# Kernel tuning notes

Measured on AMD Instinct MI355X. Metric: run time of the kernel, lower is better.

Reference implementation:

```python
import jax, jax.numpy as jnp
import numpy as np

# Model constants (match init_kwargs)
H, P, N, G, NL, K = 32, 64, 128, 1, 15, 4   # heads, head_dim, state, groups, lambda levels, conv width
HID, T, BATCH = 1024, 1024, 1
INTER = H * P                    # 2048
CONV_DIM = INTER + 2 * G * N     # 2304
PROJ = INTER + CONV_DIM + H * (NL + 1)  # 4864
EPS = 1e-5


def _level_matrix(t_len: int) -> np.ndarray:
    """Fenwick-tree level assignment: for query t, prefix [0,t] splits into
    power-of-two segments from binary expansion of t+1; segment of length 2^l -> level l."""
    lm = np.zeros((t_len, t_len), dtype=np.int32)
    for t in range(t_len):
        n = t + 1
        while n > 0:
            lb = n & (-n)
            lm[t, n - lb:n] = lb.bit_length() - 1
            n -= lb
    return lm


def setup_inputs() -> dict:
    key = jax.random.key(0)
    ks = jax.random.split(key, 4)
    return {
        "hidden_states": jax.random.normal(ks[0], (BATCH, T, HID), jnp.float32),
        "in_proj_w": jax.random.normal(ks[1], (PROJ, HID), jnp.float32) / np.sqrt(HID).astype(np.float32),
        "in_proj_b": jnp.zeros((PROJ,), jnp.float32),
        "conv_w": jax.random.normal(ks[2], (CONV_DIM, K), jnp.float32) / np.sqrt(K).astype(np.float32),
        "dt_bias": jnp.ones((H,), jnp.float32),
        "A_log": jnp.log(jnp.arange(1, H + 1, dtype=jnp.float32)),
        "L_param": jnp.ones((H, NL), jnp.float32),
        "D": jnp.ones((H,), jnp.float32),
        "rmsnorm_w": jnp.ones((INTER,), jnp.float32),
        "out_proj_w": jax.random.normal(ks[3], (HID, INTER), jnp.float32) / np.sqrt(INTER).astype(np.float32),
        "out_proj_b": jnp.zeros((HID,), jnp.float32),
        "level_mat": jnp.asarray(_level_matrix(T)),  # (T,T) int32, data-independent
    }


def reference(hidden_states, in_proj_w, in_proj_b, conv_w, dt_bias, A_log,
              L_param, D, rmsnorm_w, out_proj_w, out_proj_b, level_mat):
    b, t, _ = hidden_states.shape
    # in_proj and split: [z | xBC | dt | dl]
    zxbcdtdl = hidden_states @ in_proj_w.T + in_proj_b
    z, xBC, dt, dl = jnp.split(zxbcdtdl, [INTER, INTER + CONV_DIM, INTER + CONV_DIM + H], axis=-1)
    # depthwise causal conv1d (width K) + SiLU
    xp = jnp.pad(xBC, ((0, 0), (K - 1, 0), (0, 0)))
    conv = sum(xp[:, w:w + t, :] * conv_w[:, w] for w in range(K))
    xBC = jax.nn.silu(conv)
    x, Bm, Cm = jnp.split(xBC, [INTER, INTER + G * N], axis=-1)
    x = x.reshape(b, t, H, P)          # v pre-scale
    Bm = Bm.reshape(b, t, G, N)        # keys
    Cm = Cm.reshape(b, t, G, N)        # queries
    dl = dl.reshape(b, t, H, NL)
    # D residual uses unscaled x (matches hmamba_chunk_scan_combined ordering)
    D_res = x * D[None, None, :, None]
    dt = jax.nn.softplus(dt + dt_bias)            # (b,t,H)
    v = x * dt[..., None]                          # (b,t,H,P)
    A = -jnp.exp(A_log)                            # (H,)
    g = A * dt                                     # (b,t,H), per-token log-decay (<=0)
    Ls = jax.nn.softplus(L_param * dl)             # (b,t,H,NL) per-token level scales
    # cumulative log-decay; decay(t,s) = exp(cg_t - cg_s), s<=t
    cg = jnp.cumsum(g, axis=1).transpose(0, 2, 1)  # (b,H,t)
    mask = jnp.tril(jnp.ones((t, t), bool))
    logdecay = jnp.where(mask, cg[:, :, :, None] - cg[:, :, None, :], -jnp.inf)
    decay = jnp.exp(logdecay)                      # (b,H,t,s)
    # hierarchical level scale H[t,s] = Ls[b,t,h, level(t,s)]
    Hmat = jnp.take_along_axis(Ls.transpose(0, 2, 1, 3), level_mat[None, None, :, :], axis=-1)  # (b,H,t,s)
    scores = jnp.einsum('btgn,bsgn->bgts', Cm, Bm)  # (b,G,t,s), G=1 broadcasts over heads
    att = scores * decay * Hmat                     # (b,H,t,s), masked via decay=0
    y = jnp.einsum('bhts,bshp->bthp', att, v) + D_res
    y = y.reshape(b, t, INTER)
    # gated RMSNorm with norm_before_gate=False: normalize(y * silu(z)) * w
    yg = y * jax.nn.silu(z)
    y = yg * jax.lax.rsqrt(jnp.mean(yg * yg, axis=-1, keepdims=True) + EPS) * rmsnorm_w
    return y @ out_proj_w.T + out_proj_b
```

## Files before the change

kernel.cpp:

```cpp
#include <hip/hip_runtime.h>
#include <hip/hip_bf16.h>
#include <math.h>

#define T_LEN 1024
#define HID 1024
#define NHEAD 32
#define HDIM 64
#define NSTATE 128
#define NLVL 15
#define KCONV 4
#define INTER 2048
#define CONV_DIM 2304
#define PROJ 4864
#define EPS 1e-5f

typedef __attribute__((ext_vector_type(8))) _Float16 half8;
typedef __attribute__((ext_vector_type(4))) float float4v;
typedef unsigned short ushort_t;

__device__ __forceinline__ float softplus_f(float x) {
  return fmaxf(x, 0.f) + log1pf(expf(-fabsf(x)));
}
__device__ __forceinline__ float silu_f(float x) {
  return x / (1.f + expf(-x));
}
__device__ __forceinline__ ushort_t f2h(float f) {
  union { _Float16 h; ushort_t u; } v;
  v.h = (_Float16)f;
  return v.u;
}
__device__ __forceinline__ void gload_lds16(const void* g, void* l) {
  __builtin_amdgcn_global_load_lds(
      (const __attribute__((address_space(1))) void*)g,
      (__attribute__((address_space(3))) void*)l, 16, 0, 0);
}

__global__ __launch_bounds__(256) void f32_to_f16(const float* __restrict__ src,
                                                  ushort_t* __restrict__ dst, int n4) {
  int i = blockIdx.x * 256 + threadIdx.x;
  if (i >= n4) return;
  float4 v = reinterpret_cast<const float4*>(src)[i];
  union { ushort_t u[4]; unsigned long long ll; } o;
  o.u[0] = f2h(v.x); o.u[1] = f2h(v.y); o.u[2] = f2h(v.z); o.u[3] = f2h(v.w);
  reinterpret_cast<unsigned long long*>(dst)[i] = o.ll;
}

__global__ __launch_bounds__(256) void gemm_f16_sk(
    const ushort_t* __restrict__ A, const ushort_t* __restrict__ B,
    float* __restrict__ Cpart, int M, int N, int K, int Kc) {
  __shared__ ushort_t As[2][128][32];
  __shared__ ushort_t Bs[2][128][32];
  const int tid = threadIdx.x;
  const int w = tid >> 6, L = tid & 63;
  const int n0 = blockIdx.x * 128, m0 = blockIdx.y * 128;
  const int kbeg = blockIdx.z * Kc;
  float* __restrict__ C = Cpart + (size_t)blockIdx.z * M * N;
  const int mq = (w & 1) * 64, nq = (w >> 1) * 64;

  const int srow = (L >> 2);
  const int sch = (L & 3) * 8;

  float4v acc[4][4];
#pragma unroll
  for (int i = 0; i < 4; ++i)
#pragma unroll
    for (int j = 0; j < 4; ++j) acc[i][j] = (float4v){0.f, 0.f, 0.f, 0.f};

  const int niter = Kc / 32;
  {
    const int kk = kbeg;
#pragma unroll
    for (int j = 0; j < 2; ++j) {
      int r0 = 16 * (w * 2 + j);
      gload_lds16(A + (size_t)(m0 + r0 + srow) * K + kk + sch, &As[0][r0][0]);
      gload_lds16(B + (size_t)(n0 + r0 + srow) * K + kk + sch, &Bs[0][r0][0]);
    }
  }
  for (int it = 0; it < niter; ++it) {
    __syncthreads();
    if (it + 1 < niter) {
      const int kk = kbeg + (it + 1) * 32;
      const int nb = (it + 1) & 1;
#pragma unroll
      for (int j = 0; j < 2; ++j) {
        int r0 = 16 * (w * 2 + j);
        gload_lds16(A + (size_t)(m0 + r0 + srow) * K + kk + sch, &As[nb][r0][0]);
        gload_lds16(B + (size_t)(n0 + r0 + srow) * K + kk + sch, &Bs[nb][r0][0]);
      }
    }
    const int cb = it & 1;
    half8 af[4], bf[4];
#pragma unroll
    for (int t = 0; t < 4; ++t) {
      af[t] = *reinterpret_cast<const half8*>(&As[cb][mq + t * 16 + (L & 15)][(L >> 4) * 8]);
      bf[t] = *reinterpret_cast<const half8*>(&Bs[cb][nq + t * 16 + (L & 15)][(L >> 4) * 8]);
    }
#pragma unroll
    for (int mt = 0; mt < 4; ++mt)
#pragma unroll
      for (int nt = 0; nt < 4; ++nt)
        acc[mt][nt] = __builtin_amdgcn_mfma_f32_16x16x32_f16(af[mt], bf[nt], acc[mt][nt], 0, 0, 0);
  }
  const int qrow = (L >> 4) * 4;
#pragma unroll
  for (int mt = 0; mt < 4; ++mt) {
#pragma unroll
    for (int nt = 0; nt < 4; ++nt) {
      int col = n0 + nq + nt * 16 + (L & 15);
#pragma unroll
      for (int r = 0; r < 4; ++r) {
        int row = m0 + mq + mt * 16 + qrow + r;
        C[(size_t)row * N + col] = acc[mt][nt][r];
      }
    }
  }
}

__global__ __launch_bounds__(256) void reduce_out4(const float* __restrict__ p,
                                                   const float* __restrict__ bias,
                                                   float* __restrict__ out, int MN) {
  int i = blockIdx.x * 256 + threadIdx.x;
  if (i * 4 >= MN) return;
  float4 a = reinterpret_cast<const float4*>(p)[i];
  float4 b = reinterpret_cast<const float4*>(p + MN)[i];
  float4 c = reinterpret_cast<const float4*>(p + 2 * (size_t)MN)[i];
  float4 d = reinterpret_cast<const float4*>(p + 3 * (size_t)MN)[i];
  int col = (i * 4) & (HID - 1);
  float4 bv = *reinterpret_cast<const float4*>(bias + col);
  float4 o;
  o.x = a.x + b.x + c.x + d.x + bv.x;
  o.y = a.y + b.y + c.y + d.y + bv.y;
  o.z = a.z + b.z + c.z + d.z + bv.z;
  o.w = a.w + b.w + c.w + d.w + bv.w;
  reinterpret_cast<float4*>(out)[i] = o;
}

__global__ __launch_bounds__(512) void pointwise_dt(
    const float* __restrict__ zx0, const float* __restrict__ zx1,
    const float* __restrict__ in_b, const float* __restrict__ dt_bias,
    const float* __restrict__ A_log, const float* __restrict__ L_param,
    float* __restrict__ dtbuf, float* __restrict__ gbuf,
    float* __restrict__ Lsbuf) {
  const int t = blockIdx.x;
  const int j = threadIdx.x;
  const size_t ro = (size_t)t * PROJ;
  if (j < NHEAD * NLVL) {
    int c = INTER + CONV_DIM + NHEAD + j;
    float x = L_param[j] * (zx0[ro + c] + zx1[ro + c] + in_b[c]);
    Lsbuf[(size_t)t * (NHEAD * NLVL) + j] = softplus_f(x);
  } else {
    int h = j - NHEAD * NLVL;
    int c = INTER + CONV_DIM + h;
    float x = zx0[ro + c] + zx1[ro + c] + in_b[c] + dt_bias[h];
    float dt = softplus_f(x);
    dtbuf[t * NHEAD + h] = dt;
    gbuf[t * NHEAD + h] = -expf(A_log[h]) * dt;
  }
}

__global__ __launch_bounds__(256) void conv_silu(
    const float* __restrict__ zx0, const float* __restrict__ zx1,
    const float* __restrict__ in_b, const float* __restrict__ conv_w,
    const float* __restrict__ dtbuf, const float* __restrict__ Dp,
    ushort_t* __restrict__ vb, float* __restrict__ ybuf,
    ushort_t* __restrict__ Bb, ushort_t* __restrict__ Cb) {
  int idx = blockIdx.x * 256 + threadIdx.x;
  if (idx >= T_LEN * CONV_DIM) return;
  int t = idx / CONV_DIM;
  int c = idx - t * CONV_DIM;
  const float bc = in_b[INTER + c];
  float acc = 0.f;
#pragma unroll
  for (int w = 0; w < KCONV; ++w) {
    int tt = t - (KCONV - 1) + w;
    if (tt >= 0) {
      size_t o = (size_t)tt * PROJ + INTER + c;
      acc += (zx0[o] + zx1[o] + bc) * conv_w[c * KCONV + w];
    }
  }
  float sil = silu_f(acc);
  if (c < INTER) {
    int h = c >> 6;
    float dt = dtbuf[t * NHEAD + h];
    vb[(size_t)t * INTER + c] = f2h(sil * dt);
    ybuf[(size_t)t * INTER + c] = sil * Dp[h];
  } else if (c < INTER + NSTATE) {
    Bb[t * NSTATE + (c - INTER)] = f2h(sil);
  } else {
    Cb[t * NSTATE + (c - INTER - NSTATE)] = f2h(sil);
  }
}

__global__ __launch_bounds__(256) void vtrans(const ushort_t* __restrict__ vb,
                                              ushort_t* __restrict__ vt) {
  __shared__ ushort_t Tl[64][72];
  const int tid = threadIdx.x;
  const int t0 = blockIdx.x * 64, c0 = blockIdx.y * 64;
#pragma unroll
  for (int i = 0; i < 2; ++i) {
    int u = tid + 256 * i;
    int r = u >> 3, c8 = (u & 7) * 8;
    *reinterpret_cast<half8*>(&Tl[r][c8]) =
        *reinterpret_cast<const half8*>(vb + (size_t)(t0 + r) * INTER + c0 + c8);
  }
  __syncthreads();
#pragma unroll
  for (int i = 0; i < 2; ++i) {
    int u = tid + 256 * i;
    int p = u >> 3, t8 = (u & 7) * 8;
    union { ushort_t u16[8]; half8 h; } o;
#pragma unroll
    for (int j = 0; j < 8; ++j) o.u16[j] = Tl[t8 + j][p];
    *reinterpret_cast<half8*>(vt + (size_t)(c0 + p) * T_LEN + t0 + t8) = o.h;
  }
}

__global__ __launch_bounds__(1024) void scan_g(const float* __restrict__ gbuf,
                                               double* __restrict__ cgd) {
  __shared__ double buf[T_LEN];
  const int h = blockIdx.x, t = threadIdx.x;
  buf[t] = (double)gbuf[t * NHEAD + h];
  __syncthreads();
  for (int off = 1; off < T_LEN; off <<= 1) {
    double v = buf[t];
    double a = (t >= off) ? buf[t - off] : 0.0;
    __syncthreads();
    buf[t] = v + a;
    __syncthreads();
  }
  cgd[(size_t)h * T_LEN + t] = buf[t];
}

__global__ __launch_bounds__(256) void attn_mfma(
    const ushort_t* __restrict__ Bb, const ushort_t* __restrict__ Cb,
    const ushort_t* __restrict__ vt, const double* __restrict__ cgd,
    const float* __restrict__ Lsb, float* __restrict__ ybuf) {
  __shared__ ushort_t Bl[64][136];
  __shared__ ushort_t Vtl[64][72];
  __shared__ ushort_t Sl[64][72];
  __shared__ float Lsl[64][17];
  __shared__ float cgq[64];
  __shared__ float cgs[64];

  const int item = blockIdx.x;
  const int h = item / 40;
  const int rem = item - h * 40;
  int qt, j;
  if (rem < 4)        { qt = rem;                 j = 0; }
  else if (rem < 12)  { qt = 4 + (rem - 4) / 2;   j = (rem - 4) % 2; }
  else if (rem < 24)  { qt = 8 + (rem - 12) / 3;  j = (rem - 12) % 3; }
  else                { qt = 12 + (rem - 24) / 4; j = (rem - 24) % 4; }

  const int tid = threadIdx.x;
  const int w = tid >> 6, L = tid & 63;
  const int tq0 = qt * 64;
  const double* cgh = cgd + (size_t)h * T_LEN;
  const double base = cgh[tq0];

  for (int i = tid; i < 64 * NLVL; i += 256) {
    int r = i / NLVL, l = i - r * NLVL;
    Lsl[r][l] = Lsb[(size_t)(tq0 + r) * (NHEAD * NLVL) + h * NLVL + l];
  }
  if (tid < 64) cgq[tid] = (float)(cgh[tq0 + tid] - base);

  half8 cfrag[4];
  {
    const ushort_t* cr = Cb + (size_t)(tq0 + w * 16 + (L & 15)) * NSTATE + (L >> 4) * 8;
#pragma unroll
    for (int ks = 0; ks < 4; ++ks)
      cfrag[ks] = *reinterpret_cast<const half8*>(cr + ks * 32);
  }
  float4v yac[4];
#pragma unroll
  for (int i = 0; i < 4; ++i) yac[i] = (float4v){0.f, 0.f, 0.f, 0.f};

  const int qrow = w * 16 + ((L >> 4) << 2);

  const int st0 = 4 * j;
  const int st1 = min(4 * j + 4, qt + 1);
  for (int st = st0; st < st1; ++st) {
    const int ts0 = st * 64;
    __syncthreads();
#pragma unroll
    for (int i = 0; i < 4; ++i) {
      int u = tid + 256 * i;
      int row = u >> 4, kb = (u & 15) * 8;
      *reinterpret_cast<half8*>(&Bl[row][kb]) =
          *reinterpret_cast<const half8*>(Bb + (size_t)(ts0 + row) * NSTATE + kb);
    }
#pragma unroll
    for (int i = 0; i < 2; ++i) {
      int u = tid + 256 * i;
      int p = u >> 3, sc = (u & 7) * 8;
      *reinterpret_cast<half8*>(&Vtl[p][sc]) =
          *reinterpret_cast<const half8*>(vt + (size_t)(h * HDIM + p) * T_LEN + ts0 + sc);
    }
    if (tid < 64) cgs[tid] = (float)(cgh[ts0 + tid] - base);
    __syncthreads();

    float4v sac[4];
#pragma unroll
    for (int nt = 0; nt < 4; ++nt) sac[nt] = (float4v){0.f, 0.f, 0.f, 0.f};
#pragma unroll
    for (int ks = 0; ks < 4; ++ks) {
#pragma unroll
      for (int nt = 0; nt < 4; ++nt) {
        half8 bfrag = *reinterpret_cast<const half8*>(&Bl[nt * 16 + (L & 15)][ks * 32 + (L >> 4) * 8]);
        sac[nt] = __builtin_amdgcn_mfma_f32_16x16x32_f16(cfrag[ks], bfrag, sac[nt], 0, 0, 0);
      }
    }
#pragma unroll
    for (int nt = 0; nt < 4; ++nt) {
      int s = nt * 16 + (L & 15);
      int sg = ts0 + s;
      float cs = cgs[s];
#pragma unroll
      for (int r = 0; r < 4; ++r) {
        int q = qrow + r;
        int tg = tq0 + q;
        float val = 0.f;
        if (sg <= tg) {
          int lvl = 31 - __clz((unsigned)(sg ^ (tg + 1)));
          val = sac[nt][r] * __expf(cgq[q] - cs) * Lsl[q][lvl];
        }
        Sl[q][s] = f2h(val);
      }
    }
    __builtin_amdgcn_s_waitcnt(0);
#pragma unroll
    for (int ks = 0; ks < 2; ++ks) {
      half8 af = *reinterpret_cast<const half8*>(&Sl[w * 16 + (L & 15)][ks * 32 + (L >> 4) * 8]);
#pragma unroll
      for (int pt = 0; pt < 4; ++pt) {
        half8 bfv = *reinterpret_cast<const half8*>(&Vtl[pt * 16 + (L & 15)][ks * 32 + (L >> 4) * 8]);
        yac[pt] = __builtin_amdgcn_mfma_f32_16x16x32_f16(af, bfv, yac[pt], 0, 0, 0);
      }
    }
  }
#pragma unroll
  for (int pt = 0; pt < 4; ++pt) {
    int p = pt * 16 + (L & 15);
#pragma unroll
    for (int r = 0; r < 4; ++r) {
      int q = qrow + r;
      atomicAdd(ybuf + (size_t)(tq0 + q) * INTER + h * HDIM + p, yac[pt][r]);
    }
  }
}

__global__ __launch_bounds__(256) void rmsnorm_gate(
    const float* __restrict__ ybuf, const float* __restrict__ zx0,
    const float* __restrict__ zx1, const float* __restrict__ in_b,
    const float* __restrict__ w, ushort_t* __restrict__ yhf) {
  __shared__ float red[4];
  const int t = blockIdx.x, tid = threadIdx.x;
  const size_t ro = (size_t)t * PROJ;
  const float* yrow = ybuf + (size_t)t * INTER;
  float yg[8];
  float ss = 0.f;
#pragma unroll
  for (int i = 0; i < 8; ++i) {
    int c = tid + 256 * i;
    float z = zx0[ro + c] + zx1[ro + c] + in_b[c];
    float g = yrow[c] * silu_f(z);
    yg[i] = g;
    ss += g * g;
  }
#pragma unroll
  for (int off = 32; off; off >>= 1) ss += __shfl_down(ss, off, 64);
  if ((tid & 63) == 0) red[tid >> 6] = ss;
  __syncthreads();
  if (tid == 0) red[0] = red[0] + red[1] + red[2] + red[3];
  __syncthreads();
  const float scale = rsqrtf(red[0] / (float)INTER + EPS);
#pragma unroll
  for (int i = 0; i < 8; ++i) {
    int c = tid + 256 * i;
    yhf[(size_t)t * INTER + c] = f2h(yg[i] * scale * w[c]);
  }
}

extern "C" void kernel_launch(void* const* d_in, const int* in_sizes, int n_in,
                              void* d_out, int out_size, void* d_ws, size_t ws_size,
                              hipStream_t stream) {
  const float* hs        = (const float*)d_in[0];
  const float* in_proj_w = (const float*)d_in[1];
  const float* in_proj_b = (const float*)d_in[2];
  const float* conv_w    = (const float*)d_in[3];
  const float* dt_bias   = (const float*)d_in[4];
  const float* A_log     = (const float*)d_in[5];
  const float* L_param   = (const float*)d_in[6];
  const float* Dp        = (const float*)d_in[7];
  const float* rms_w     = (const float*)d_in[8];
  const float* out_proj_w= (const float*)d_in[9];
  const float* out_proj_b= (const float*)d_in[10];
  float* out = (float*)d_out;

  char* W = (char*)d_ws;
  size_t off = 0;
  auto alloc = [&](size_t bytes) { void* p = W + off; off = (off + bytes + 255) & ~(size_t)255; return p; };
  double*   cgd = (double*)  alloc((size_t)NHEAD * T_LEN * 8);
  float*    zx0 = (float*)   alloc((size_t)T_LEN * PROJ * 4);
  float*    zx1 = (float*)   alloc((size_t)T_LEN * PROJ * 4);
  float*    opp = (float*)   alloc((size_t)4 * T_LEN * HID * 4);
  float*    ybuf= (float*)   alloc((size_t)T_LEN * INTER * 4);
  float*    gbuf= (float*)   alloc((size_t)T_LEN * NHEAD * 4);
  float*    dtb = (float*)   alloc((size_t)T_LEN * NHEAD * 4);
  float*    Lsb = (float*)   alloc((size_t)T_LEN * NHEAD * NLVL * 4);
  ushort_t* hsb = (ushort_t*)alloc((size_t)T_LEN * HID * 2);
  ushort_t* Wib = (ushort_t*)alloc((size_t)PROJ * HID * 2);
  ushort_t* Wob = (ushort_t*)alloc((size_t)HID * INTER * 2);
  ushort_t* yhf = (ushort_t*)alloc((size_t)T_LEN * INTER * 2);
  ushort_t* vb  = (ushort_t*)alloc((size_t)T_LEN * INTER * 2);
  ushort_t* vt  = (ushort_t*)alloc((size_t)T_LEN * INTER * 2);
  ushort_t* Bb  = (ushort_t*)alloc((size_t)T_LEN * NSTATE * 2);
  ushort_t* Cb  = (ushort_t*)alloc((size_t)T_LEN * NSTATE * 2);

  f32_to_f16<<<(T_LEN * HID / 4 + 255) / 256, 256, 0, stream>>>(hs, hsb, T_LEN * HID / 4);
  f32_to_f16<<<(PROJ * HID / 4 + 255) / 256, 256, 0, stream>>>(in_proj_w, Wib, PROJ * HID / 4);
  f32_to_f16<<<(HID * INTER / 4 + 255) / 256, 256, 0, stream>>>(out_proj_w, Wob, HID * INTER / 4);

  gemm_f16_sk<<<dim3(PROJ / 128, T_LEN / 128, 2), 256, 0, stream>>>(
      hsb, Wib, zx0, T_LEN, PROJ, HID, HID / 2);

  pointwise_dt<<<T_LEN, 512, 0, stream>>>(zx0, zx1, in_proj_b, dt_bias, A_log, L_param,
                                          dtb, gbuf, Lsb);

  conv_silu<<<(T_LEN * CONV_DIM + 255) / 256, 256, 0, stream>>>(
      zx0, zx1, in_proj_b, conv_w, dtb, Dp, vb, ybuf, Bb, Cb);

  vtrans<<<dim3(T_LEN / 64, INTER / 64), 256, 0, stream>>>(vb, vt);

  scan_g<<<NHEAD, T_LEN, 0, stream>>>(gbuf, cgd);

  attn_mfma<<<NHEAD * 40, 256, 0, stream>>>(Bb, Cb, vt, cgd, Lsb, ybuf);

  rmsnorm_gate<<<T_LEN, 256, 0, stream>>>(ybuf, zx0, zx1, in_proj_b, rms_w, yhf);

  gemm_f16_sk<<<dim3(HID / 128, T_LEN / 128, 4), 256, 0, stream>>>(
      yhf, Wob, opp, T_LEN, HID, INTER, INTER / 4);
  reduce_out4<<<(T_LEN * HID / 4 + 255) / 256, 256, 0, stream>>>(
      opp, out_proj_b, out, T_LEN * HID);
}
```

Before: 211.3 us.

## Fuse f16 conversions, fold V transpose into conv, and rewrite scan as wavefront

```diff
diff --git a/kernel.cpp b/kernel.cpp
--- a/kernel.cpp
+++ b/kernel.cpp
@@ -35,14 +35,22 @@
       (__attribute__((address_space(3))) void*)l, 16, 0, 0);
 }
 
-__global__ __launch_bounds__(256) void f32_to_f16(const float* __restrict__ src,
-                                                  ushort_t* __restrict__ dst, int n4) {
+#define N4_HS  (T_LEN * HID / 4)
+#define N4_WI  (PROJ * HID / 4)
+#define N4_WO  (HID * INTER / 4)
+__global__ __launch_bounds__(256) void prep_f16(
+    const float* __restrict__ hs, const float* __restrict__ wi,
+    const float* __restrict__ wo, ushort_t* __restrict__ hsb,
+    ushort_t* __restrict__ wib, ushort_t* __restrict__ wob) {
   int i = blockIdx.x * 256 + threadIdx.x;
-  if (i >= n4) return;
-  float4 v = reinterpret_cast<const float4*>(src)[i];
+  const float* src; ushort_t* dst; int j;
+  if (i < N4_HS)              { src = hs; dst = hsb; j = i; }
+  else if (i < N4_HS + N4_WI) { src = wi; dst = wib; j = i - N4_HS; }
+  else                        { src = wo; dst = wob; j = i - N4_HS - N4_WI; }
+  float4 v = reinterpret_cast<const float4*>(src)[j];
   union { ushort_t u[4]; unsigned long long ll; } o;
   o.u[0] = f2h(v.x); o.u[1] = f2h(v.y); o.u[2] = f2h(v.z); o.u[3] = f2h(v.w);
-  reinterpret_cast<unsigned long long*>(dst)[i] = o.ll;
+  reinterpret_cast<unsigned long long*>(dst)[j] = o.ll;
 }
 
 __global__ __launch_bounds__(256) void gemm_f16_sk(
@@ -56,7 +64,6 @@
   const int kbeg = blockIdx.z * Kc;
   float* __restrict__ C = Cpart + (size_t)blockIdx.z * M * N;
   const int mq = (w & 1) * 64, nq = (w >> 1) * 64;
-
   const int srow = (L >> 2);
   const int sch = (L & 3) * 8;
 
@@ -139,7 +146,7 @@
     const float* __restrict__ zx0, const float* __restrict__ zx1,
     const float* __restrict__ in_b, const float* __restrict__ dt_bias,
     const float* __restrict__ A_log, const float* __restrict__ L_param,
-    float* __restrict__ dtbuf, float* __restrict__ gbuf,
+    float* __restrict__ dtbuf, float* __restrict__ gT,
     float* __restrict__ Lsbuf) {
   const int t = blockIdx.x;
   const int j = threadIdx.x;
@@ -154,81 +161,90 @@
     float x = zx0[ro + c] + zx1[ro + c] + in_b[c] + dt_bias[h];
     float dt = softplus_f(x);
     dtbuf[t * NHEAD + h] = dt;
-    gbuf[t * NHEAD + h] = -expf(A_log[h]) * dt;
-  }
-}
-
-__global__ __launch_bounds__(256) void conv_silu(
+    gT[h * T_LEN + t] = -expf(A_log[h]) * dt;
+  }
+}
+
+__global__ __launch_bounds__(64) void scan_g(const float* __restrict__ gT,
+                                             double* __restrict__ cgd) {
+  const int h = blockIdx.x, l = threadIdx.x;
+  const float* gr = gT + (size_t)h * T_LEN + l * 16;
+  double pre[16];
+  double acc = 0.0;
+#pragma unroll
+  for (int i = 0; i < 16; ++i) { acc += (double)gr[i]; pre[i] = acc; }
+  double s = acc;
+#pragma unroll
+  for (int off = 1; off < 64; off <<= 1) {
+    double o = __shfl_up(s, off, 64);
+    if (l >= off) s += o;
+  }
+  const double base = s - acc;
+  double* cr = cgd + (size_t)h * T_LEN + l * 16;
+#pragma unroll
+  for (int i = 0; i < 16; ++i) cr[i] = base + pre[i];
+}
+
+__global__ __launch_bounds__(256) void conv_fused(
     const float* __restrict__ zx0, const float* __restrict__ zx1,
     const float* __restrict__ in_b, const float* __restrict__ conv_w,
     const float* __restrict__ dtbuf, const float* __restrict__ Dp,
-    ushort_t* __restrict__ vb, float* __restrict__ ybuf,
+    ushort_t* __restrict__ vt, float* __restrict__ ybuf,
     ushort_t* __restrict__ Bb, ushort_t* __restrict__ Cb) {
-  int idx = blockIdx.x * 256 + threadIdx.x;
-  if (idx >= T_LEN * CONV_DIM) return;
-  int t = idx / CONV_DIM;
-  int c = idx - t * CONV_DIM;
-  const float bc = in_b[INTER + c];
-  float acc = 0.f;
-#pragma unroll
-  for (int w = 0; w < KCONV; ++w) {
-    int tt = t - (KCONV - 1) + w;
+  __shared__ ushort_t Vl[64][68];
+  __shared__ float dtl[64];
+  const int tq = blockIdx.x, cy = blockIdx.y;
+  const int t0 = tq * 64;
+  const int tid = threadIdx.x;
+  const int lane = tid & 63, g = tid >> 6;
+  const bool vpath = (cy < 32);
+  const int ccol = vpath ? cy * 64 + lane : INTER + (cy - 32) * 64 + lane;
+  const int zcol = INTER + ccol;
+  float cw[KCONV];
+#pragma unroll
+  for (int w = 0; w < KCONV; ++w) cw[w] = conv_w[ccol * KCONV + w];
+  const float bc = in_b[zcol];
+  if (vpath && tid < 64) dtl[tid] = dtbuf[(t0 + tid) * NHEAD + cy];
+  const float Dh = vpath ? Dp[cy] : 0.f;
+
+  float xv[19];
+#pragma unroll
+  for (int i = 0; i < 19; ++i) {
+    int tt = t0 + g * 16 - 3 + i;
     if (tt >= 0) {
-      size_t o = (size_t)tt * PROJ + INTER + c;
-      acc += (zx0[o] + zx1[o] + bc) * conv_w[c * KCONV + w];
-    }
-  }
-  float sil = silu_f(acc);
-  if (c < INTER) {
-    int h = c >> 6;
-    float dt = dtbuf[t * NHEAD + h];
-    vb[(size_t)t * INTER + c] = f2h(sil * dt);
-    ybuf[(size_t)t * INTER + c] = sil * Dp[h];
-  } else if (c < INTER + NSTATE) {
-    Bb[t * NSTATE + (c - INTER)] = f2h(sil);
-  } else {
-    Cb[t * NSTATE + (c - INTER - NSTATE)] = f2h(sil);
-  }
-}
-
-__global__ __launch_bounds__(256) void vtrans(const ushort_t* __restrict__ vb,
-                                              ushort_t* __restrict__ vt) {
-  __shared__ ushort_t Tl[64][72];
-  const int tid = threadIdx.x;
-  const int t0 = blockIdx.x * 64, c0 = blockIdx.y * 64;
-#pragma unroll
-  for (int i = 0; i < 2; ++i) {
-    int u = tid + 256 * i;
-    int r = u >> 3, c8 = (u & 7) * 8;
-    *reinterpret_cast<half8*>(&Tl[r][c8]) =
-        *reinterpret_cast<const half8*>(vb + (size_t)(t0 + r) * INTER + c0 + c8);
+      size_t o = (size_t)tt * PROJ + zcol;
+      xv[i] = zx0[o] + zx1[o] + bc;
+    } else xv[i] = 0.f;
   }
   __syncthreads();
 #pragma unroll
-  for (int i = 0; i < 2; ++i) {
-    int u = tid + 256 * i;
-    int p = u >> 3, t8 = (u & 7) * 8;
-    union { ushort_t u16[8]; half8 h; } o;
-#pragma unroll
-    for (int j = 0; j < 8; ++j) o.u16[j] = Tl[t8 + j][p];
-    *reinterpret_cast<half8*>(vt + (size_t)(c0 + p) * T_LEN + t0 + t8) = o.h;
-  }
-}
-
-__global__ __launch_bounds__(1024) void scan_g(const float* __restrict__ gbuf,
-                                               double* __restrict__ cgd) {
-  __shared__ double buf[T_LEN];
-  const int h = blockIdx.x, t = threadIdx.x;
-  buf[t] = (double)gbuf[t * NHEAD + h];
-  __syncthreads();
-  for (int off = 1; off < T_LEN; off <<= 1) {
-    double v = buf[t];
-    double a = (t >= off) ? buf[t - off] : 0.0;
+  for (int i = 0; i < 16; ++i) {
+    float acc = xv[i] * cw[0] + xv[i + 1] * cw[1] + xv[i + 2] * cw[2] + xv[i + 3] * cw[3];
+    float sil = silu_f(acc);
+    int tl = g * 16 + i;
+    int t = t0 + tl;
+    if (vpath) {
+      ushort_t vh = f2h(sil * dtl[tl]);
+      Vl[tl][lane] = vh;
+      ybuf[(size_t)t * INTER + cy * 64 + lane] = sil * Dh;
+    } else if (ccol < INTER + NSTATE) {
+      Bb[t * NSTATE + (ccol - INTER)] = f2h(sil);
+    } else {
+      Cb[t * NSTATE + (ccol - INTER - NSTATE)] = f2h(sil);
+    }
+  }
+  if (vpath) {
     __syncthreads();
-    buf[t] = v + a;
-    __syncthreads();
-  }
-  cgd[(size_t)h * T_LEN + t] = buf[t];
+#pragma unroll
+    for (int rep = 0; rep < 2; ++rep) {
+      int u = tid + 256 * rep;
+      int p = u >> 3, t8 = (u & 7) * 8;
+      union { ushort_t u16[8]; half8 h; } o;
+#pragma unroll
+      for (int j = 0; j < 8; ++j) o.u16[j] = Vl[t8 + j][p];
+      *reinterpret_cast<half8*>(vt + (size_t)(cy * 64 + p) * T_LEN + t0 + t8) = o.h;
+    }
+  }
 }
 
 __global__ __launch_bounds__(256) void attn_mfma(
@@ -238,7 +254,7 @@
   __shared__ ushort_t Bl[64][136];
   __shared__ ushort_t Vtl[64][72];
   __shared__ ushort_t Sl[64][72];
-  __shared__ float Lsl[64][17];
+  __shared__ float Lsl[64][16];
   __shared__ float cgq[64];
   __shared__ float cgs[64];
 
@@ -404,34 +420,30 @@
   float*    zx1 = (float*)   alloc((size_t)T_LEN * PROJ * 4);
   float*    opp = (float*)   alloc((size_t)4 * T_LEN * HID * 4);
   float*    ybuf= (float*)   alloc((size_t)T_LEN * INTER * 4);
-  float*    gbuf= (float*)   alloc((size_t)T_LEN * NHEAD * 4);
+  float*    gT  = (float*)   alloc((size_t)NHEAD * T_LEN * 4);
   float*    dtb = (float*)   alloc((size_t)T_LEN * NHEAD * 4);
   float*    Lsb = (float*)   alloc((size_t)T_LEN * NHEAD * NLVL * 4);
   ushort_t* hsb = (ushort_t*)alloc((size_t)T_LEN * HID * 2);
   ushort_t* Wib = (ushort_t*)alloc((size_t)PROJ * HID * 2);
   ushort_t* Wob = (ushort_t*)alloc((size_t)HID * INTER * 2);
   ushort_t* yhf = (ushort_t*)alloc((size_t)T_LEN * INTER * 2);
-  ushort_t* vb  = (ushort_t*)alloc((size_t)T_LEN * INTER * 2);
   ushort_t* vt  = (ushort_t*)alloc((size_t)T_LEN * INTER * 2);
   ushort_t* Bb  = (ushort_t*)alloc((size_t)T_LEN * NSTATE * 2);
   ushort_t* Cb  = (ushort_t*)alloc((size_t)T_LEN * NSTATE * 2);
 
-  f32_to_f16<<<(T_LEN * HID / 4 + 255) / 256, 256, 0, stream>>>(hs, hsb, T_LEN * HID / 4);
-  f32_to_f16<<<(PROJ * HID / 4 + 255) / 256, 256, 0, stream>>>(in_proj_w, Wib, PROJ * HID / 4);
-  f32_to_f16<<<(HID * INTER / 4 + 255) / 256, 256, 0, stream>>>(out_proj_w, Wob, HID * INTER / 4);
+  prep_f16<<<(N4_HS + N4_WI + N4_WO) / 256, 256, 0, stream>>>(
+      hs, in_proj_w, out_proj_w, hsb, Wib, Wob);
 
   gemm_f16_sk<<<dim3(PROJ / 128, T_LEN / 128, 2), 256, 0, stream>>>(
       hsb, Wib, zx0, T_LEN, PROJ, HID, HID / 2);
 
   pointwise_dt<<<T_LEN, 512, 0, stream>>>(zx0, zx1, in_proj_b, dt_bias, A_log, L_param,
-                                          dtb, gbuf, Lsb);
-
-  conv_silu<<<(T_LEN * CONV_DIM + 255) / 256, 256, 0, stream>>>(
-      zx0, zx1, in_proj_b, conv_w, dtb, Dp, vb, ybuf, Bb, Cb);
-
-  vtrans<<<dim3(T_LEN / 64, INTER / 64), 256, 0, stream>>>(vb, vt);
-
-  scan_g<<<NHEAD, T_LEN, 0, stream>>>(gbuf, cgd);
+                                          dtb, gT, Lsb);
+
+  scan_g<<<NHEAD, 64, 0, stream>>>(gT, cgd);
+
+  conv_fused<<<dim3(T_LEN / 64, 36), 256, 0, stream>>>(
+      zx0, zx1, in_proj_b, conv_w, dtb, Dp, vt, ybuf, Bb, Cb);
 
   attn_mfma<<<NHEAD * 40, 256, 0, stream>>>(Bb, Cb, vt, cgd, Lsb, ybuf);
 
```

New measurement: 200.2 us. -5.2%, faster.
